# Performance work log

Hardware: AMD Instinct MI355X
Metric: run time of the kernel (lower is better)

The kernel has to match this reference:

```python
import jax, jax.numpy as jnp
import numpy as np

N_NODES = 100000
N_FEAT = 128
N_EDGES = 640000
BATCH_SIZE = 50000


def setup_inputs() -> dict:
    key = jax.random.key(0)
    k1, k2 = jax.random.split(key)
    x = jax.random.normal(k1, (N_NODES, N_FEAT), dtype=jnp.float32)
    edge_index = jax.random.randint(k2, (2, N_EDGES), 0, N_NODES, dtype=jnp.int32)
    return {"x": x, "edge_index": edge_index, "batch_size": BATCH_SIZE}


def reference(x, edge_index, batch_size):
    # Filter edges whose destination is inside the target batch, then
    # scatter-sum source node features into destination rows (SpMM with a
    # 0/1 adjacency), matching adj.t().matmul(x) in the original.
    src = edge_index[0]
    dst = edge_index[1]
    valid = dst < batch_size                                  # [E]
    # Route invalid edges to a dummy segment (batch_size) and zero their values.
    seg = jnp.where(valid, dst, batch_size)                   # [E]
    vals = x[src] * valid[:, None].astype(x.dtype)            # [E, F] gather
    x_neighbors_sum = jax.ops.segment_sum(
        vals, seg, num_segments=batch_size + 1)[:batch_size]  # [B, F]
    node_labels = jnp.concatenate(
        [x[:batch_size, :], x_neighbors_sum], axis=-1)        # [B, 2F]
    return node_labels
```

## Files before the change

kernel.cpp:

```cpp
#include <hip/hip_runtime.h>

#define NFEAT 128
#define CAP 32
#define OVF_CAP 4096

typedef float nfloat4 __attribute__((ext_vector_type(4)));


__global__ void zero_kernel(int* __restrict__ p, int n) {
    int t = blockIdx.x * blockDim.x + threadIdx.x;
    if (t < n) p[t] = 0;
}

__global__ void bin_kernel(const int* __restrict__ src, const int* __restrict__ dst,
                           int* __restrict__ cnt, int* __restrict__ ovf_cnt,
                           int* __restrict__ ovf, int* __restrict__ bucket,
                           int E, int B) {
    int t = blockIdx.x * blockDim.x + threadIdx.x;
    int e0 = t << 2;
    if (e0 >= E) return;
    int s[4], d[4];
    int m;
    if (e0 + 4 <= E) {
        m = 4;
        int4 sv = *(const int4*)(src + e0);
        int4 dv = *(const int4*)(dst + e0);
        s[0] = sv.x; s[1] = sv.y; s[2] = sv.z; s[3] = sv.w;
        d[0] = dv.x; d[1] = dv.y; d[2] = dv.z; d[3] = dv.w;
    } else {
        m = E - e0;
        for (int i = 0; i < m; ++i) { s[i] = src[e0 + i]; d[i] = dst[e0 + i]; }
    }
    #pragma unroll
    for (int i = 0; i < 4; ++i) {
        if (i >= m) break;
        int dd = d[i];
        if (dd >= B) continue;
        int pos = atomicAdd(&cnt[dd], 1);
        if (pos < CAP) {
            bucket[dd * CAP + pos] = s[i];
        } else {
            int o = atomicAdd(ovf_cnt, 1);
            if (o < OVF_CAP) { ovf[2 * o] = s[i]; ovf[2 * o + 1] = dd; }
        }
    }
}

__global__ void bin_kernel_scalar(const int* __restrict__ src, const int* __restrict__ dst,
                                  int* __restrict__ cnt, int* __restrict__ ovf_cnt,
                                  int* __restrict__ ovf, int* __restrict__ bucket,
                                  int E, int B) {
    int e = blockIdx.x * blockDim.x + threadIdx.x;
    if (e >= E) return;
    int dd = dst[e];
    if (dd >= B) return;
    int pos = atomicAdd(&cnt[dd], 1);
    if (pos < CAP) bucket[dd * CAP + pos] = src[e];
    else { int o = atomicAdd(ovf_cnt, 1); if (o < OVF_CAP) { ovf[2 * o] = src[e]; ovf[2 * o + 1] = dd; } }
}

__global__ __launch_bounds__(256, 8)
void aggregate_kernel(const float4* __restrict__ x4,
                      const int* __restrict__ cnt,
                      const int* __restrict__ bucket,
                      const int* __restrict__ ovf_cnt,
                      const int* __restrict__ ovf,
                      float4* __restrict__ out4, int B) {
    int wid = (blockIdx.x * blockDim.x + threadIdx.x) >> 6;
    int lane = threadIdx.x & 63;
    int half = lane >> 5;
    int c = lane & 31;
    int bl = half << 5;
    int w = (wid << 1) + half;
    bool rv = (w < B);
    int wv = rv ? w : 0;
    int k = cnt[wv];
    if (k > CAP) k = CAP;
    if (!rv) k = 0;
    int ko = __shfl(k, lane ^ 32, 64);
    int km = (k > ko) ? k : ko;
    int sid = (c < k) ? bucket[wv * CAP + c] : 0;
    float4 xd = x4[(size_t)wv * 32 + c];
    float4 acc = make_float4(0.f, 0.f, 0.f, 0.f);
    int kc = (k > 0) ? (k - 1) : 0;
    for (int j = 0; j < km; j += 8) {
        int   idx[8];
        float msk[8];
        #pragma unroll
        for (int i = 0; i < 8; ++i) {
            int jj = j + i;
            int jc = (jj < kc) ? jj : kc;
            idx[i] = __shfl(sid, bl + jc, 64);
            msk[i] = (jj < k) ? 1.f : 0.f;
        }
        float4 v[8];
        #pragma unroll
        for (int i = 0; i < 8; ++i) v[i] = x4[(size_t)idx[i] * 32 + c];
        #pragma unroll
        for (int i = 0; i < 8; ++i) {
            acc.x = fmaf(msk[i], v[i].x, acc.x);
            acc.y = fmaf(msk[i], v[i].y, acc.y);
            acc.z = fmaf(msk[i], v[i].z, acc.z);
            acc.w = fmaf(msk[i], v[i].w, acc.w);
        }
    }
    int n = *ovf_cnt;
    if (n > OVF_CAP) n = OVF_CAP;
    for (int i = 0; i < n; ++i) {
        if (rv && ovf[2 * i + 1] == w) {
            float4 v = x4[(size_t)ovf[2 * i] * 32 + c];
            acc.x += v.x; acc.y += v.y; acc.z += v.z; acc.w += v.w;
        }
    }
    if (rv) {
        size_t o = (size_t)w * 64;
        nfloat4 xv = { xd.x, xd.y, xd.z, xd.w };
        nfloat4 av = { acc.x, acc.y, acc.z, acc.w };
        __builtin_nontemporal_store(xv, (nfloat4*)&out4[o + c]);
        __builtin_nontemporal_store(av, (nfloat4*)&out4[o + 32 + c]);
    }
}

__global__ void init_out_kernel(const float4* __restrict__ x4,
                                float4* __restrict__ out4, int B) {
    int t = blockIdx.x * blockDim.x + threadIdx.x;
    if (t >= B * 64) return;
    int row = t >> 6, c = t & 63;
    float4 v = (c < 32) ? x4[(size_t)row * 32 + c] : make_float4(0.f, 0.f, 0.f, 0.f);
    out4[t] = v;
}

__global__ void edge_scatter_atomic_kernel(const float* __restrict__ x,
                                           const int* __restrict__ src,
                                           const int* __restrict__ dst,
                                           float* __restrict__ out, int E, int B) {
    int t = blockIdx.x * blockDim.x + threadIdx.x;
    int e = t >> 5;
    if (e >= E) return;
    int d = dst[e];
    if (d >= B) return;
    int c = t & 31;
    const float4 v = ((const float4*)(x + (size_t)src[e] * NFEAT))[c];
    float* o = out + (size_t)d * 256 + NFEAT + c * 4;
    unsafeAtomicAdd(o + 0, v.x);
    unsafeAtomicAdd(o + 1, v.y);
    unsafeAtomicAdd(o + 2, v.z);
    unsafeAtomicAdd(o + 3, v.w);
}

extern "C" void kernel_launch(void* const* d_in, const int* in_sizes, int n_in,
                              void* d_out, int out_size, void* d_ws, size_t ws_size,
                              hipStream_t stream) {
    const float* x  = (const float*)d_in[0];
    const int*   ei = (const int*)d_in[1];
    const int E = in_sizes[1] / 2;
    const int B = out_size / (2 * NFEAT);
    float* out = (float*)d_out;
    const int* src = ei;
    const int* dst = ei + E;

    size_t need = ((size_t)B * (CAP + 1) + 1 + 2 * OVF_CAP) * sizeof(int);
    if (ws_size >= need) {
        int* cnt     = (int*)d_ws;
        int* ovf_cnt = cnt + B;
        int* ovf     = ovf_cnt + 1;
        int* bucket  = ovf + 2 * OVF_CAP;

        int nz = B + 1;
        zero_kernel<<<(nz + 255) / 256, 256, 0, stream>>>(cnt, nz);
        if ((E & 3) == 0) {
            int nt = E / 4;
            bin_kernel<<<(nt + 255) / 256, 256, 0, stream>>>(
                src, dst, cnt, ovf_cnt, ovf, bucket, E, B);
        } else {
            bin_kernel_scalar<<<(E + 255) / 256, 256, 0, stream>>>(
                src, dst, cnt, ovf_cnt, ovf, bucket, E, B);
        }
        int waves = (B + 1) / 2;
        aggregate_kernel<<<(waves + 3) / 4, 256, 0, stream>>>(
            (const float4*)x, cnt, bucket, ovf_cnt, ovf, (float4*)out, B);
    } else {
        init_out_kernel<<<(B * 64 + 255) / 256, 256, 0, stream>>>(
            (const float4*)x, (float4*)out, B);
        long long total = (long long)E * 32;
        edge_scatter_atomic_kernel<<<(int)((total + 255) / 256), 256, 0, stream>>>(
            x, src, dst, out, E, B);
    }
}
```

Baseline: 147.8 us.

## Move x-copy half of output into binning kernel, drop nontemporal stores

The binning kernel now also copies x[:B] into the first half of each output row, using a grid-stride loop. The aggregate kernel then writes only the neighbor-sum half. The intent is to overlap the bandwidth-heavy copy with the atomic-bound binning and to remove the extra row load from aggregation. The change also drops the nontemporal stores and the launch_bounds hint, and removes the scalar binning path, so inputs with E not divisible by 4 now take the slow atomic fallback.

```diff
diff --git a/kernel.cpp b/kernel.cpp
--- a/kernel.cpp
+++ b/kernel.cpp
@@ -3,8 +3,6 @@
 #define NFEAT 128
 #define CAP 32
 #define OVF_CAP 4096
-
-typedef float nfloat4 __attribute__((ext_vector_type(4)));
 
 
 __global__ void zero_kernel(int* __restrict__ p, int n) {
@@ -15,21 +13,28 @@
 __global__ void bin_kernel(const int* __restrict__ src, const int* __restrict__ dst,
                            int* __restrict__ cnt, int* __restrict__ ovf_cnt,
                            int* __restrict__ ovf, int* __restrict__ bucket,
-                           int E, int B) {
+                           const float4* __restrict__ x4, float4* __restrict__ out4,
+                           int E, int B, int nthreads) {
     int t = blockIdx.x * blockDim.x + threadIdx.x;
     int e0 = t << 2;
-    if (e0 >= E) return;
     int s[4], d[4];
-    int m;
-    if (e0 + 4 <= E) {
-        m = 4;
-        int4 sv = *(const int4*)(src + e0);
-        int4 dv = *(const int4*)(dst + e0);
-        s[0] = sv.x; s[1] = sv.y; s[2] = sv.z; s[3] = sv.w;
-        d[0] = dv.x; d[1] = dv.y; d[2] = dv.z; d[3] = dv.w;
-    } else {
-        m = E - e0;
-        for (int i = 0; i < m; ++i) { s[i] = src[e0 + i]; d[i] = dst[e0 + i]; }
+    int m = 0;
+    if (e0 < E) {
+        if (e0 + 4 <= E) {
+            m = 4;
+            int4 sv = *(const int4*)(src + e0);
+            int4 dv = *(const int4*)(dst + e0);
+            s[0] = sv.x; s[1] = sv.y; s[2] = sv.z; s[3] = sv.w;
+            d[0] = dv.x; d[1] = dv.y; d[2] = dv.z; d[3] = dv.w;
+        } else {
+            m = E - e0;
+            for (int i = 0; i < m; ++i) { s[i] = src[e0 + i]; d[i] = dst[e0 + i]; }
+        }
+    }
+    int total4 = B * 32;
+    for (int i = t; i < total4; i += nthreads) {
+        int row = i >> 5, c = i & 31;
+        out4[(size_t)row * 64 + c] = x4[(size_t)row * 32 + c];
     }
     #pragma unroll
     for (int i = 0; i < 4; ++i) {
@@ -46,26 +51,12 @@
     }
 }
 
-__global__ void bin_kernel_scalar(const int* __restrict__ src, const int* __restrict__ dst,
-                                  int* __restrict__ cnt, int* __restrict__ ovf_cnt,
-                                  int* __restrict__ ovf, int* __restrict__ bucket,
-                                  int E, int B) {
-    int e = blockIdx.x * blockDim.x + threadIdx.x;
-    if (e >= E) return;
-    int dd = dst[e];
-    if (dd >= B) return;
-    int pos = atomicAdd(&cnt[dd], 1);
-    if (pos < CAP) bucket[dd * CAP + pos] = src[e];
-    else { int o = atomicAdd(ovf_cnt, 1); if (o < OVF_CAP) { ovf[2 * o] = src[e]; ovf[2 * o + 1] = dd; } }
-}
-
-__global__ __launch_bounds__(256, 8)
-void aggregate_kernel(const float4* __restrict__ x4,
-                      const int* __restrict__ cnt,
-                      const int* __restrict__ bucket,
-                      const int* __restrict__ ovf_cnt,
-                      const int* __restrict__ ovf,
-                      float4* __restrict__ out4, int B) {
+__global__ void aggregate_kernel(const float4* __restrict__ x4,
+                                 const int* __restrict__ cnt,
+                                 const int* __restrict__ bucket,
+                                 const int* __restrict__ ovf_cnt,
+                                 const int* __restrict__ ovf,
+                                 float4* __restrict__ out4, int B) {
     int wid = (blockIdx.x * blockDim.x + threadIdx.x) >> 6;
     int lane = threadIdx.x & 63;
     int half = lane >> 5;
@@ -80,7 +71,6 @@
     int ko = __shfl(k, lane ^ 32, 64);
     int km = (k > ko) ? k : ko;
     int sid = (c < k) ? bucket[wv * CAP + c] : 0;
-    float4 xd = x4[(size_t)wv * 32 + c];
     float4 acc = make_float4(0.f, 0.f, 0.f, 0.f);
     int kc = (k > 0) ? (k - 1) : 0;
     for (int j = 0; j < km; j += 8) {
@@ -113,11 +103,7 @@
         }
     }
     if (rv) {
-        size_t o = (size_t)w * 64;
-        nfloat4 xv = { xd.x, xd.y, xd.z, xd.w };
-        nfloat4 av = { acc.x, acc.y, acc.z, acc.w };
-        __builtin_nontemporal_store(xv, (nfloat4*)&out4[o + c]);
-        __builtin_nontemporal_store(av, (nfloat4*)&out4[o + 32 + c]);
+        out4[(size_t)w * 64 + 32 + c] = acc;
     }
 }
 
@@ -160,7 +146,7 @@
     const int* dst = ei + E;
 
     size_t need = ((size_t)B * (CAP + 1) + 1 + 2 * OVF_CAP) * sizeof(int);
-    if (ws_size >= need) {
+    if (ws_size >= need && (E & 3) == 0) {
         int* cnt     = (int*)d_ws;
         int* ovf_cnt = cnt + B;
         int* ovf     = ovf_cnt + 1;
@@ -168,14 +154,11 @@
 
         int nz = B + 1;
         zero_kernel<<<(nz + 255) / 256, 256, 0, stream>>>(cnt, nz);
-        if ((E & 3) == 0) {
-            int nt = E / 4;
-            bin_kernel<<<(nt + 255) / 256, 256, 0, stream>>>(
-                src, dst, cnt, ovf_cnt, ovf, bucket, E, B);
-        } else {
-            bin_kernel_scalar<<<(E + 255) / 256, 256, 0, stream>>>(
-                src, dst, cnt, ovf_cnt, ovf, bucket, E, B);
-        }
+        int nt = E / 4;
+        int nblocks = (nt + 255) / 256;
+        bin_kernel<<<nblocks, 256, 0, stream>>>(
+            src, dst, cnt, ovf_cnt, ovf, bucket,
+            (const float4*)x, (float4*)out, E, B, nblocks * 256);
         int waves = (B + 1) / 2;
         aggregate_kernel<<<(waves + 3) / 4, 256, 0, stream>>>(
             (const float4*)x, cnt, bucket, ovf_cnt, ovf, (float4*)out, B);
```

Result: faster. 141.2 us (-4.5%).
